# Performance work log

Hardware: AMD Instinct MI355X
Metric: run time of the kernel (lower is better)

The kernel has to match this reference:

```python
import jax, jax.numpy as jnp
import numpy as np
from jax import lax

TOP_N = 4
CAT_NUM = 4
IOU_THRESH = 0.25
PAD = 224
OUT_SZ = 224


def _gen_edge_anchors():
    # Faithful port of NTSNet._generate_default_anchor_maps for 448x448 input.
    settings = (
        dict(stride=32, size=48, scale=[2 ** (1.0 / 3.0), 2 ** (2.0 / 3.0)], ar=[0.667, 1, 1.5]),
        dict(stride=64, size=96, scale=[2 ** (1.0 / 3.0), 2 ** (2.0 / 3.0)], ar=[0.667, 1, 1.5]),
        dict(stride=128, size=192, scale=[1, 2 ** (1.0 / 3.0), 2 ** (2.0 / 3.0)], ar=[0.667, 1, 1.5]),
    )
    inp = np.array([448, 448], dtype=np.float32)
    edges = []
    for s in settings:
        stride = s['stride']
        oh, ow = np.ceil(inp / stride).astype(int)
        ostart = stride / 2.0
        oy = np.arange(ostart, ostart + stride * oh, stride, dtype=np.float32).reshape(oh, 1)
        ox = np.arange(ostart, ostart + stride * ow, stride, dtype=np.float32).reshape(1, ow)
        cy = np.broadcast_to(oy, (oh, ow)); cx = np.broadcast_to(ox, (oh, ow))
        for sc in s['scale']:
            for ar in s['ar']:
                h = s['size'] * sc / float(ar) ** 0.5
                w = s['size'] * sc * float(ar) ** 0.5
                e = np.stack([cy - h / 2.0, cx - w / 2.0, cy + h / 2.0, cx + w / 2.0], axis=-1).reshape(-1, 4)
                edges.append(e)
    return np.concatenate(edges, 0).astype(np.float32)

EDGE_ANCHORS = (_gen_edge_anchors() + PAD).astype(np.int32)  # [1614,4] (y0,x0,y1,x1) in padded coords
BOXES_F = jnp.asarray(EDGE_ANCHORS, jnp.float32)
BOXES_I = jnp.asarray(EDGE_ANCHORS, jnp.int32)
AREAS = (BOXES_F[:, 2] - BOXES_F[:, 0]) * (BOXES_F[:, 3] - BOXES_F[:, 1])
N_ANCHORS = EDGE_ANCHORS.shape[0]  # 1614


def _nms_single(scores):
    # Greedy hard NMS: pick top score, suppress IoU >= thresh, repeat TOP_N times.
    def step(valid, _):
        s = jnp.where(valid, scores, -jnp.inf)
        i = jnp.argmax(s)
        b = BOXES_F[i]
        sy = jnp.maximum(BOXES_F[:, 0], b[0]); sx = jnp.maximum(BOXES_F[:, 1], b[1])
        ey = jnp.minimum(BOXES_F[:, 2], b[2]); ex = jnp.minimum(BOXES_F[:, 3], b[3])
        ly = ey - sy; lx = ex - sx
        inter = jnp.where((ly < 0) | (lx < 0), 0.0, ly * lx)
        iou = inter / (AREAS + AREAS[i] - inter)
        return valid & (iou < IOU_THRESH), i
    _, idx = lax.scan(step, jnp.ones((N_ANCHORS,), bool), None, length=TOP_N)
    return idx  # [TOP_N] int


def _crop_resize(img, box):
    # img: [3, 896, 896]; box: int [4] = (y0,x0,y1,x1); bilinear, align_corners=True -> [3,224,224]
    hmax = img.shape[-1] - 1
    y0, x0, y1, x1 = box[0], box[1], box[2], box[3]
    t = jnp.arange(OUT_SZ, dtype=jnp.float32) / (OUT_SZ - 1.0)
    ys = y0.astype(jnp.float32) + t * (y1 - y0 - 1).astype(jnp.float32)
    xs = x0.astype(jnp.float32) + t * (x1 - x0 - 1).astype(jnp.float32)
    yf = jnp.floor(ys); xf = jnp.floor(xs)
    wy = (ys - yf)[None, :, None]; wx = (xs - xf)[None, None, :]
    yl = yf.astype(jnp.int32); yh = jnp.minimum(yl + 1, hmax)
    xl = xf.astype(jnp.int32); xh = jnp.minimum(xl + 1, hmax)
    g = lambda yi, xi: img[:, yi[:, None], xi[None, :]]
    top = g(yl, xl) * (1.0 - wx) + g(yl, xh) * wx
    bot = g(yh, xl) * (1.0 - wx) + g(yh, xh) * wx
    return top * (1.0 - wy) + bot * wy


def _conv(x, w, b, stride, pad):
    y = lax.conv_general_dilated(x, w, (stride, stride), ((pad, pad), (pad, pad)),
                                 dimension_numbers=('NCHW', 'OIHW', 'NCHW'))
    return y + b[None, :, None, None]


def _forward(x, bb_w, bb_b, w1, b1, t1w, t1b, w2, b2, t2w, t2b, w3, b3, t3w, t3b, cw, cb):
    B = x.shape[0]
    backbone = lambda z: jax.nn.relu(_conv(z, bb_w, bb_b, 32, 0))
    raw_pre = backbone(x)  # [B,2048,14,14]
    # Navigator unit
    y1 = jax.nn.relu(_conv(raw_pre, w1, b1, 1, 1))                                  # [B,128,14,14]
    z1 = (jnp.einsum('bchw,oc->bohw', y1, t1w) + t1b[None, :, None, None]).reshape(B, -1)
    y2 = jax.nn.relu(_conv(y1, w2, b2, 2, 1))                                        # [B,128,7,7]
    z2 = (jnp.einsum('bchw,oc->bohw', y2, t2w) + t2b[None, :, None, None]).reshape(B, -1)
    y3 = jax.nn.relu(_conv(y2, w3, b3, 2, 1))                                        # [B,128,4,4]
    z3 = (jnp.einsum('bchw,oc->bohw', y3, t3w) + t3b[None, :, None, None]).reshape(B, -1)
    rpn_score = jnp.concatenate([z1, z2, z3], axis=1)  # [B,1614]
    top_idx = jax.vmap(_nms_single)(rpn_score)          # [B,TOP_N]
    boxes = BOXES_I[top_idx]                            # [B,TOP_N,4]
    x_pad = jnp.pad(x, ((0, 0), (0, 0), (PAD, PAD), (PAD, PAD)))  # [B,3,896,896]
    parts = jax.vmap(lambda img, bs: jax.vmap(lambda b: _crop_resize(img, b))(bs))(x_pad, boxes)
    parts = lax.stop_gradient(parts).reshape(B * TOP_N, 3, OUT_SZ, OUT_SZ)  # .detach() in torch
    part_feat = backbone(parts).mean(axis=(2, 3)).reshape(B, TOP_N, 2048)
    part_feat = part_feat[:, :CAT_NUM].reshape(B, -1)   # [B,8192]
    raw_feat = lax.stop_gradient(raw_pre).mean(axis=(2, 3))  # [B,2048] (detached in torch)
    concat = jnp.concatenate([part_feat, raw_feat], axis=1)  # [B,10240]
    return concat @ cw.T + cb                           # [B,200]


def setup_inputs() -> dict:
    key = jax.random.key(0)
    ks = jax.random.split(key, 12)
    def w(k, shape, fan_in):
        return jax.random.normal(k, shape, jnp.float32) * np.float32(np.sqrt(2.0 / fan_in))
    return {
        'x': jax.random.normal(ks[0], (8, 3, 448, 448), jnp.float32),
        'bb_w': w(ks[1], (2048, 3, 32, 32), 3 * 32 * 32), 'bb_b': jnp.zeros((2048,), jnp.float32),
        'w1': w(ks[2], (128, 2048, 3, 3), 2048 * 9), 'b1': jnp.zeros((128,), jnp.float32),
        't1w': w(ks[3], (6, 128), 128), 't1b': jnp.zeros((6,), jnp.float32),
        'w2': w(ks[4], (128, 128, 3, 3), 128 * 9), 'b2': jnp.zeros((128,), jnp.float32),
        't2w': w(ks[5], (6, 128), 128), 't2b': jnp.zeros((6,), jnp.float32),
        'w3': w(ks[6], (128, 128, 3, 3), 128 * 9), 'b3': jnp.zeros((128,), jnp.float32),
        't3w': w(ks[7], (9, 128), 128), 't3b': jnp.zeros((9,), jnp.float32),
        'cw': w(ks[8], (200, 2048 * (CAT_NUM + 1)), 2048 * (CAT_NUM + 1)),
        'cb': jnp.zeros((200,), jnp.float32),
    }


def reference(x, bb_w, bb_b, w1, b1, t1w, t1b, w2, b2, t2w, t2b, w3, b3, t3w, t3b, cw, cb):
    return _forward(x, bb_w, bb_b, w1, b1, t1w, t1b, w2, b2, t2w, t2b, w3, b3, t3w, t3b, cw, cb)
```

## Files before the change

kernel.cpp:

```cpp
#include <hip/hip_runtime.h>
#include <math.h>


typedef _Float16 h8 __attribute__((ext_vector_type(8)));
typedef float f32x4 __attribute__((ext_vector_type(4)));

#define ASCALE 256.0f
#define WSCALE 16384.0f
#define RSCALE (1.0f / (256.0f * 16384.0f))

__device__ __forceinline__ void gload16(const void* g, void* l) {
  __builtin_amdgcn_global_load_lds(
      (__attribute__((address_space(1))) void*)(void*)(uintptr_t)g,
      (__attribute__((address_space(3))) void*)l, 16, 0, 0);
}

__global__ __launch_bounds__(256) void anchors_kernel(int* __restrict__ anch,
                                                      float* __restrict__ areas) {
  int i = blockIdx.x * 256 + threadIdx.x;
  if (i >= 1614) return;
  int stride, oh, a, pos;
  double size, sc;
  const double C13 = 1.2599210498948732;
  const double C23 = 1.5874010519681994;
  if (i < 1176) {
    stride = 32; size = 48.0; oh = 14; a = i / 196; pos = i % 196;
    sc = (a / 3 == 0) ? C13 : C23;
  } else if (i < 1470) {
    int r = i - 1176; stride = 64; size = 96.0; oh = 7; a = r / 49; pos = r % 49;
    sc = (a / 3 == 0) ? C13 : C23;
  } else {
    int r = i - 1470; stride = 128; size = 192.0; oh = 4; a = r / 16; pos = r % 16;
    int si = a / 3;
    sc = (si == 0) ? 1.0 : ((si == 1) ? C13 : C23);
  }
  int ari = a % 3;
  double ar = (ari == 0) ? 0.667 : ((ari == 1) ? 1.0 : 1.5);
  int gy = pos / oh, gx = pos % oh;
  float cy = 0.5f * (float)stride + (float)(stride * gy);
  float cx = 0.5f * (float)stride + (float)(stride * gx);
  double ss = sqrt(ar);
  double hd = (size * sc) / ss;
  double wd = (size * sc) * ss;
  float hh = (float)(hd * 0.5), wh = (float)(wd * 0.5);
  float e0 = (cy - hh) + 224.0f;
  float e1 = (cx - wh) + 224.0f;
  float e2 = (cy + hh) + 224.0f;
  float e3 = (cx + wh) + 224.0f;
  int y0 = (int)e0, x0 = (int)e1, y1i = (int)e2, x1i = (int)e3;
  anch[i * 4 + 0] = y0; anch[i * 4 + 1] = x0;
  anch[i * 4 + 2] = y1i; anch[i * 4 + 3] = x1i;
  areas[i] = (float)(y1i - y0) * (float)(x1i - x0);
}

__global__ __launch_bounds__(256) void permute_w(const float* __restrict__ w,
                                                 float* __restrict__ wp,
                                                 int Cout, int Cin) {
  int idx = blockIdx.x * 256 + threadIdx.x;
  int total = Cout * 9 * Cin;
  if (idx >= total) return;
  int c = idx % Cin; int t2 = idx / Cin; int tap = t2 % 9; int o = t2 / 9;
  wp[idx] = w[(o * Cin + c) * 9 + tap];
}

__global__ __launch_bounds__(256) void split_w(const float* __restrict__ src,
                                               _Float16* __restrict__ h,
                                               _Float16* __restrict__ l, int n8) {
  int i = blockIdx.x * 256 + threadIdx.x;
  if (i >= n8) return;
  float4 v0 = *(const float4*)(src + (size_t)i * 8);
  float4 v1 = *(const float4*)(src + (size_t)i * 8 + 4);
  float vv[8] = {v0.x, v0.y, v0.z, v0.w, v1.x, v1.y, v1.z, v1.w};
  h8 vh, vl;
#pragma unroll
  for (int j = 0; j < 8; ++j) {
    float s = vv[j] * WSCALE;
    _Float16 a = (_Float16)s;
    vh[j] = a; vl[j] = (_Float16)(s - (float)a);
  }
  *(h8*)(h + (size_t)i * 8) = vh;
  *(h8*)(l + (size_t)i * 8) = vl;
}

__global__ __launch_bounds__(256) void split_x(const float* __restrict__ x,
                                               _Float16* __restrict__ Ah,
                                               _Float16* __restrict__ Al) {
  int i = blockIdx.x * 256 + threadIdx.x;
  if (i >= 1664 * 384) return;
  int kq = i % 384, m = i / 384;
  int k = kq * 8;
  h8 vh = {}, vl = {};
  if (m < 1568) {
    int b = m / 196, pos = m % 196;
    int c = k >> 10, r = (k >> 5) & 31, col = k & 31;
    int py = (pos / 14) * 32 + r, px = (pos % 14) * 32 + col;
    const float* sp2 = x + (((size_t)(b * 3 + c) * 448 + py) * 448 + px);
    float4 v0 = *(const float4*)sp2;
    float4 v1 = *(const float4*)(sp2 + 4);
    float vv[8] = {v0.x, v0.y, v0.z, v0.w, v1.x, v1.y, v1.z, v1.w};
#pragma unroll
    for (int j = 0; j < 8; ++j) {
      float s = vv[j] * ASCALE;
      _Float16 a = (_Float16)s;
      vh[j] = a; vl[j] = (_Float16)(s - (float)a);
    }
  }
  *(h8*)(Ah + (size_t)m * 3072 + k) = vh;
  *(h8*)(Al + (size_t)m * 3072 + k) = vl;
}

__global__ __launch_bounds__(256) void gemm_bb_mfma(
    const _Float16* __restrict__ Ah, const _Float16* __restrict__ Al,
    const _Float16* __restrict__ Bh, const _Float16* __restrict__ Bl,
    float* __restrict__ P) {
  __shared__ __align__(16) char lds[32768];
  const int t = threadIdx.x;
  const int m0 = blockIdx.x * 128, n0 = blockIdx.y * 128;
  const int kz = blockIdx.z;
  const int lane = t & 63, w = t >> 6;
  const int wm = (w >> 1) * 64, wn = (w & 1) * 64;
  const int lrow = lane & 15, kg = lane >> 4;

  int offA[4], offB[4];
#pragma unroll
  for (int i = 0; i < 4; ++i) {
    int ba = (wm + i * 16 + lrow) * 64 + kg * 16;
    offA[i] = ba ^ (((ba >> 7) & 3) << 4);
    int bb2 = (wn + i * 16 + lrow) * 64 + kg * 16;
    offB[i] = bb2 ^ (((bb2 >> 7) & 3) << 4);
  }
  size_t gAo[2], gBo[2];
  int ldso[2];
#pragma unroll
  for (int e = 0; e < 2; ++e) {
    int p = e * 256 + t;
    int lsl = p ^ ((p >> 3) & 3);
    int row = lsl >> 2, kq = lsl & 3;
    gAo[e] = (size_t)(m0 + row) * 3072 + kq * 8;
    gBo[e] = (size_t)(n0 + row) * 3072 + kq * 8;
    ldso[e] = e * 4096 + (t & 192) * 16;
  }

  f32x4 acc[4][4] = {};
  const int kbeg = kz * 1536, kend = kbeg + 1536;
  for (int k0 = kbeg; k0 < kend; k0 += 32) {
#pragma unroll
    for (int e = 0; e < 2; ++e) {
      gload16(Ah + gAo[e] + k0, lds + ldso[e]);
      gload16(Al + gAo[e] + k0, lds + 8192 + ldso[e]);
      gload16(Bh + gBo[e] + k0, lds + 16384 + ldso[e]);
      gload16(Bl + gBo[e] + k0, lds + 24576 + ldso[e]);
    }
    __syncthreads();
    h8 fah[4], fal[4], fbh[4], fbl[4];
#pragma unroll
    for (int i = 0; i < 4; ++i) {
      fah[i] = *(const h8*)(lds + offA[i]);
      fal[i] = *(const h8*)(lds + 8192 + offA[i]);
      fbh[i] = *(const h8*)(lds + 16384 + offB[i]);
      fbl[i] = *(const h8*)(lds + 24576 + offB[i]);
    }
#pragma unroll
    for (int i = 0; i < 4; ++i)
#pragma unroll
      for (int j = 0; j < 4; ++j)
        acc[i][j] = __builtin_amdgcn_mfma_f32_16x16x32_f16(fah[i], fbh[j], acc[i][j], 0, 0, 0);
#pragma unroll
    for (int i = 0; i < 4; ++i)
#pragma unroll
      for (int j = 0; j < 4; ++j)
        acc[i][j] = __builtin_amdgcn_mfma_f32_16x16x32_f16(fah[i], fbl[j], acc[i][j], 0, 0, 0);
#pragma unroll
    for (int i = 0; i < 4; ++i)
#pragma unroll
      for (int j = 0; j < 4; ++j)
        acc[i][j] = __builtin_amdgcn_mfma_f32_16x16x32_f16(fal[i], fbh[j], acc[i][j], 0, 0, 0);
    __syncthreads();
  }
  float* Pz = P + (size_t)kz * 1664 * 2048;
  const int prow = (lane >> 4) * 4;
#pragma unroll
  for (int i = 0; i < 4; ++i) {
#pragma unroll
    for (int j = 0; j < 4; ++j) {
      int n = n0 + wn + j * 16 + lrow;
#pragma unroll
      for (int r = 0; r < 4; ++r) {
        int m = m0 + wm + i * 16 + prow + r;
        Pz[(size_t)m * 2048 + n] = acc[i][j][r];
      }
    }
  }
}

template <int WRITE_SPLIT>
__global__ __launch_bounds__(256) void bb_reduce(const float* __restrict__ P,
                                                 const float* __restrict__ bias,
                                                 float* __restrict__ raw,
                                                 _Float16* __restrict__ h,
                                                 _Float16* __restrict__ l) {
  int idx = blockIdx.x * 256 + threadIdx.x;
  int m = idx >> 8, col = (idx & 255) * 8;
  if (WRITE_SPLIT) {
    if (m >= 1664) return;
    if (m >= 1568) {
      h8 z = {};
      *(h8*)(h + (size_t)m * 2048 + col) = z;
      *(h8*)(l + (size_t)m * 2048 + col) = z;
      return;
    }
  } else {
    if (m >= 1568) return;
  }
  size_t o = (size_t)m * 2048 + col;
  const float* p0 = P + o;
  const float* p1 = P + (size_t)1664 * 2048 + o;
  float4 a0 = *(const float4*)(p0);
  float4 a1 = *(const float4*)(p0 + 4);
  float4 c0 = *(const float4*)(p1);
  float4 c1 = *(const float4*)(p1 + 4);
  float4 b0 = *(const float4*)(bias + col);
  float4 b1 = *(const float4*)(bias + col + 4);
  float v[8];
  v[0] = fmaxf(fmaf(a0.x + c0.x, RSCALE, b0.x), 0.f);
  v[1] = fmaxf(fmaf(a0.y + c0.y, RSCALE, b0.y), 0.f);
  v[2] = fmaxf(fmaf(a0.z + c0.z, RSCALE, b0.z), 0.f);
  v[3] = fmaxf(fmaf(a0.w + c0.w, RSCALE, b0.w), 0.f);
  v[4] = fmaxf(fmaf(a1.x + c1.x, RSCALE, b1.x), 0.f);
  v[5] = fmaxf(fmaf(a1.y + c1.y, RSCALE, b1.y), 0.f);
  v[6] = fmaxf(fmaf(a1.z + c1.z, RSCALE, b1.z), 0.f);
  v[7] = fmaxf(fmaf(a1.w + c1.w, RSCALE, b1.w), 0.f);
  *(float4*)(raw + o) = make_float4(v[0], v[1], v[2], v[3]);
  *(float4*)(raw + o + 4) = make_float4(v[4], v[5], v[6], v[7]);
  if (WRITE_SPLIT) {
    h8 vh, vl;
#pragma unroll
    for (int j = 0; j < 8; ++j) {
      float s = v[j] * ASCALE;
      _Float16 a = (_Float16)s;
      vh[j] = a; vl[j] = (_Float16)(s - (float)a);
    }
    *(h8*)(h + o) = vh;
    *(h8*)(l + o) = vl;
  }
}

__global__ __launch_bounds__(256) void gemm_nav_mfma(
    const _Float16* __restrict__ Ah, const _Float16* __restrict__ Al,
    const _Float16* __restrict__ Bh, const _Float16* __restrict__ Bl,
    float* __restrict__ part) {
  __shared__ __align__(16) char lds[32768];
  const int t = threadIdx.x;
  const int m0 = blockIdx.x * 128;
  const int sp = blockIdx.y;
  const int lane = t & 63, w = t >> 6;
  const int wm = (w >> 1) * 64, wn = (w & 1) * 64;
  const int lrow = lane & 15, kg = lane >> 4;

  int offA[4], offB[4];
#pragma unroll
  for (int i = 0; i < 4; ++i) {
    int ba = (wm + i * 16 + lrow) * 64 + kg * 16;
    offA[i] = ba ^ (((ba >> 7) & 3) << 4);
    int bb2 = (wn + i * 16 + lrow) * 64 + kg * 16;
    offB[i] = bb2 ^ (((bb2 >> 7) & 3) << 4);
  }
  size_t gBo[2];
  int ldso[2], akq8[2], ab[2], apy[2], apx[2], amv[2];
#pragma unroll
  for (int e = 0; e < 2; ++e) {
    int p = e * 256 + t;
    int lsl = p ^ ((p >> 3) & 3);
    int row = lsl >> 2, kq = lsl & 3;
    gBo[e] = (size_t)row * 18432 + kq * 8;
    ldso[e] = e * 4096 + (t & 192) * 16;
    int m = m0 + row;
    amv[e] = (m < 1568);
    int b = m / 196, pos = m % 196;
    ab[e] = b; apy[e] = pos / 14; apx[e] = pos % 14;
    akq8[e] = kq * 8;
  }

  f32x4 acc[4][4] = {};
  const int kbeg = sp * 576, kend = kbeg + 576;
  for (int k0 = kbeg; k0 < kend; k0 += 32) {
    const int tap = k0 >> 11;
    const int c = k0 & 2047;
    const int dy = tap / 3 - 1, dx = tap % 3 - 1;
#pragma unroll
    for (int e = 0; e < 2; ++e) {
      int sy = apy[e] + dy, sx = apx[e] + dx;
      bool ok = amv[e] && ((unsigned)sy < 14u) && ((unsigned)sx < 14u);
      size_t rowi = ok ? (size_t)(ab[e] * 196 + sy * 14 + sx) : (size_t)1600;
      size_t ao = rowi * 2048 + c + akq8[e];
      gload16(Ah + ao, lds + ldso[e]);
      gload16(Al + ao, lds + 8192 + ldso[e]);
      gload16(Bh + gBo[e] + k0, lds + 16384 + ldso[e]);
      gload16(Bl + gBo[e] + k0, lds + 24576 + ldso[e]);
    }
    __syncthreads();
    h8 fah[4], fal[4], fbh[4], fbl[4];
#pragma unroll
    for (int i = 0; i < 4; ++i) {
      fah[i] = *(const h8*)(lds + offA[i]);
      fal[i] = *(const h8*)(lds + 8192 + offA[i]);
      fbh[i] = *(const h8*)(lds + 16384 + offB[i]);
      fbl[i] = *(const h8*)(lds + 24576 + offB[i]);
    }
#pragma unroll
    for (int i = 0; i < 4; ++i)
#pragma unroll
      for (int j = 0; j < 4; ++j)
        acc[i][j] = __builtin_amdgcn_mfma_f32_16x16x32_f16(fah[i], fbh[j], acc[i][j], 0, 0, 0);
#pragma unroll
    for (int i = 0; i < 4; ++i)
#pragma unroll
      for (int j = 0; j < 4; ++j)
        acc[i][j] = __builtin_amdgcn_mfma_f32_16x16x32_f16(fah[i], fbl[j], acc[i][j], 0, 0, 0);
#pragma unroll
    for (int i = 0; i < 4; ++i)
#pragma unroll
      for (int j = 0; j < 4; ++j)
        acc[i][j] = __builtin_amdgcn_mfma_f32_16x16x32_f16(fal[i], fbh[j], acc[i][j], 0, 0, 0);
    __syncthreads();
  }
  const int prow = (lane >> 4) * 4;
#pragma unroll
  for (int i = 0; i < 4; ++i) {
#pragma unroll
    for (int j = 0; j < 4; ++j) {
      int n = wn + j * 16 + lrow;
#pragma unroll
      for (int r = 0; r < 4; ++r) {
        int m = m0 + wm + i * 16 + prow + r;
        if (m < 1568)
          part[((size_t)sp * 1568 + m) * 128 + n] = acc[i][j][r] * RSCALE;
      }
    }
  }
}

__global__ __launch_bounds__(256) void y1_reduce(const float* __restrict__ part,
                                                 const float* __restrict__ b1,
                                                 float* __restrict__ y1) {
  int idx = blockIdx.x * 256 + threadIdx.x;
  if (idx >= 1568 * 128) return;
  int o = idx & 127;
  float s = b1[o];
#pragma unroll
  for (int sp = 0; sp < 32; ++sp) s += part[(size_t)sp * 1568 * 128 + idx];
  y1[idx] = fmaxf(s, 0.f);
}

__global__ __launch_bounds__(256) void conv3x3s2(const float* __restrict__ in,
                                                 const float* __restrict__ wp,
                                                 const float* __restrict__ bias,
                                                 float* __restrict__ out,
                                                 int Hin, int Hout) {
  int idx = blockIdx.x * 256 + threadIdx.x;
  int total = 8 * Hout * Hout * 128;
  if (idx >= total) return;
  int o = idx & 127; int pos = idx >> 7;
  int ox = pos % Hout; int t2 = pos / Hout; int oy = t2 % Hout; int b = t2 / Hout;
  float acc = bias[o];
  for (int dy = 0; dy < 3; ++dy) {
    int iy = 2 * oy - 1 + dy;
    if (iy < 0 || iy >= Hin) continue;
    for (int dx = 0; dx < 3; ++dx) {
      int ix = 2 * ox - 1 + dx;
      if (ix < 0 || ix >= Hin) continue;
      const float* ip = in + ((b * Hin + iy) * Hin + ix) * 128;
      const float* wgt = wp + (o * 9 + dy * 3 + dx) * 128;
#pragma unroll 4
      for (int c = 0; c < 128; c += 4) {
        float4 a = *(const float4*)(ip + c);
        float4 ww = *(const float4*)(wgt + c);
        acc += a.x * ww.x + a.y * ww.y + a.z * ww.z + a.w * ww.w;
      }
    }
  }
  out[idx] = fmaxf(acc, 0.f);
}

__global__ __launch_bounds__(256) void scores_kernel(
    const float* __restrict__ y1, const float* __restrict__ y2,
    const float* __restrict__ y3, const float* __restrict__ t1w,
    const float* __restrict__ t1b, const float* __restrict__ t2w,
    const float* __restrict__ t2b, const float* __restrict__ t3w,
    const float* __restrict__ t3b, float* __restrict__ scores) {
  int idx = blockIdx.x * 256 + threadIdx.x;
  if (idx >= 8 * 1614) return;
  int b = idx / 1614, sI = idx % 1614;
  const float* f; const float* w; float bias;
  if (sI < 1176) {
    int a = sI / 196;
    f = y1 + (b * 196 + (sI % 196)) * 128; w = t1w + a * 128; bias = t1b[a];
  } else if (sI < 1470) {
    int r = sI - 1176; int a = r / 49;
    f = y2 + (b * 49 + (r % 49)) * 128; w = t2w + a * 128; bias = t2b[a];
  } else {
    int r = sI - 1470; int a = r / 16;
    f = y3 + (b * 16 + (r % 16)) * 128; w = t3w + a * 128; bias = t3b[a];
  }
  float acc = 0.f;
  for (int c = 0; c < 128; c += 4) {
    float4 a4 = *(const float4*)(f + c);
    float4 w4 = *(const float4*)(w + c);
    acc += a4.x * w4.x + a4.y * w4.y + a4.z * w4.z + a4.w * w4.w;
  }
  scores[idx] = acc + bias;
}

__global__ __launch_bounds__(256) void nms_kernel(const float* __restrict__ scores,
                                                  const int* __restrict__ anch,
                                                  const float* __restrict__ areas,
                                                  int* __restrict__ boxes) {
  const int b = blockIdx.x, t = threadIdx.x;
  const float* s = scores + b * 1614;
  __shared__ unsigned char valid[1614];
  __shared__ float rv[256];
  __shared__ int ri[256];
  for (int i = t; i < 1614; i += 256) valid[i] = 1;
  __syncthreads();
  for (int n = 0; n < 4; ++n) {
    float best = -INFINITY; int bi = 0x7fffffff;
    for (int i = t; i < 1614; i += 256) {
      if (valid[i]) {
        float v = s[i];
        if (v > best || (v == best && i < bi)) { best = v; bi = i; }
      }
    }
    rv[t] = best; ri[t] = bi;
    __syncthreads();
    for (int off = 128; off > 0; off >>= 1) {
      if (t < off) {
        float ov = rv[t + off]; int oi = ri[t + off];
        if (ov > rv[t] || (ov == rv[t] && oi < ri[t])) { rv[t] = ov; ri[t] = oi; }
      }
      __syncthreads();
    }
    int sel = ri[0];
    if (sel > 1613) sel = 0;
    const int4 bb = ((const int4*)anch)[sel];
    const float Ai = areas[sel];
    if (t == 0) ((int4*)boxes)[b * 4 + n] = bb;
    __syncthreads();
    for (int i = t; i < 1614; i += 256) {
      if (!valid[i]) continue;
      const int4 ab = ((const int4*)anch)[i];
      float sy = fmaxf((float)ab.x, (float)bb.x);
      float sx = fmaxf((float)ab.y, (float)bb.y);
      float ey = fminf((float)ab.z, (float)bb.z);
      float ex = fminf((float)ab.w, (float)bb.w);
      float ly = ey - sy, lx = ex - sx;
      float inter = (ly < 0.f || lx < 0.f) ? 0.f : ly * lx;
      float iou = inter / (areas[i] + Ai - inter);
      if (iou >= 0.25f) valid[i] = 0;
    }
    __syncthreads();
  }
}

__global__ __launch_bounds__(256) void crop_kernel(const float* __restrict__ x,
                                                   const int* __restrict__ boxes,
                                                   _Float16* __restrict__ Ah,
                                                   _Float16* __restrict__ Al) {
  int idx = blockIdx.x * 256 + threadIdx.x;
  if (idx >= 32 * 3 * 224 * 224) return;
  int px = idx % 224; int t1 = idx / 224; int py = t1 % 224; int t2 = t1 / 224;
  int c = t2 % 3; int p = t2 / 3;
  int b = p >> 2;
  const int4 bb = ((const int4*)boxes)[p];
  float ty = (float)py / 223.0f;
  float txf = (float)px / 223.0f;
  float ys = (float)bb.x + ty * (float)(bb.z - bb.x - 1);
  float xs = (float)bb.y + txf * (float)(bb.w - bb.y - 1);
  float yf = floorf(ys), xf = floorf(xs);
  float wy = ys - yf, wx = xs - xf;
  int yl = (int)yf, xl = (int)xf;
  int yh = min(yl + 1, 895), xh = min(xl + 1, 895);
  const float* img = x + (size_t)(b * 3 + c) * 448 * 448;
  auto samp = [&](int yy, int xx) -> float {
    yy -= 224; xx -= 224;
    if (yy < 0 || yy >= 448 || xx < 0 || xx >= 448) return 0.f;
    return img[yy * 448 + xx];
  };
  float v00 = samp(yl, xl), v01 = samp(yl, xh);
  float v10 = samp(yh, xl), v11 = samp(yh, xh);
  float top = v00 * (1.f - wx) + v01 * wx;
  float bot = v10 * (1.f - wx) + v11 * wx;
  float val = top * (1.f - wy) + bot * wy;
  int i = py >> 5, r = py & 31, j = px >> 5, col = px & 31;
  int m = p * 49 + i * 7 + j;
  int k = (c << 10) + (r << 5) + col;
  float s = val * ASCALE;
  _Float16 a = (_Float16)s;
  Ah[(size_t)m * 3072 + k] = a;
  Al[(size_t)m * 3072 + k] = (_Float16)(s - (float)a);
}

__global__ __launch_bounds__(256) void mean_kernel(const float* __restrict__ in,
                                                   float* __restrict__ out,
                                                   int rows) {
  int g = blockIdx.x >> 3;
  int o = ((blockIdx.x & 7) << 8) + threadIdx.x;
  const float* base = in + ((size_t)g * rows) * 2048 + o;
  float s0 = 0.f, s1 = 0.f, s2 = 0.f, s3 = 0.f;
  int r = 0;
  for (; r + 4 <= rows; r += 4) {
    s0 += base[(size_t)(r + 0) * 2048];
    s1 += base[(size_t)(r + 1) * 2048];
    s2 += base[(size_t)(r + 2) * 2048];
    s3 += base[(size_t)(r + 3) * 2048];
  }
  for (; r < rows; ++r) s0 += base[(size_t)r * 2048];
  out[(size_t)g * 2048 + o] = ((s0 + s1) + (s2 + s3)) / (float)rows;
}

__global__ __launch_bounds__(256) void final_kernel(const float* __restrict__ pfeat,
                                                    const float* __restrict__ rfeat,
                                                    const float* __restrict__ cw,
                                                    const float* __restrict__ cb,
                                                    float* __restrict__ out) {
  int gw = (blockIdx.x * 256 + threadIdx.x) >> 6;
  int lane = threadIdx.x & 63;
  if (gw >= 1600) return;
  int b = gw / 200, j = gw % 200;
  const float* wr = cw + (size_t)j * 10240;
  const float* pf = pfeat + (size_t)b * 8192;
  float acc = 0.f;
  for (int k = lane * 4; k < 8192; k += 256) {
    float4 a = *(const float4*)(pf + k);
    float4 w = *(const float4*)(wr + k);
    acc += a.x * w.x + a.y * w.y + a.z * w.z + a.w * w.w;
  }
  const float* rf = rfeat + (size_t)b * 2048;
  const float* wr2 = wr + 8192;
  for (int k = lane * 4; k < 2048; k += 256) {
    float4 a = *(const float4*)(rf + k);
    float4 w = *(const float4*)(wr2 + k);
    acc += a.x * w.x + a.y * w.y + a.z * w.z + a.w * w.w;
  }
#pragma unroll
  for (int off = 32; off > 0; off >>= 1) acc += __shfl_down(acc, off, 64);
  if (lane == 0) out[b * 200 + j] = acc + cb[j];
}

extern "C" void kernel_launch(void* const* d_in, const int* in_sizes, int n_in,
                              void* d_out, int out_size, void* d_ws, size_t ws_size,
                              hipStream_t stream) {
  const float* x   = (const float*)d_in[0];
  const float* bbw = (const float*)d_in[1];
  const float* bbb = (const float*)d_in[2];
  const float* w1  = (const float*)d_in[3];
  const float* b1  = (const float*)d_in[4];
  const float* t1w = (const float*)d_in[5];
  const float* t1b = (const float*)d_in[6];
  const float* w2  = (const float*)d_in[7];
  const float* b2  = (const float*)d_in[8];
  const float* t2w = (const float*)d_in[9];
  const float* t2b = (const float*)d_in[10];
  const float* w3  = (const float*)d_in[11];
  const float* b3  = (const float*)d_in[12];
  const float* t3w = (const float*)d_in[13];
  const float* t3b = (const float*)d_in[14];
  const float* cw  = (const float*)d_in[15];
  const float* cb  = (const float*)d_in[16];
  float* out = (float*)d_out;

  char* p = (char*)d_ws;
  auto alloc = [&](size_t bytes) -> char* {
    char* r = p; p += (bytes + 255) & ~(size_t)255; return r;
  };
  int*      anch  = (int*)     alloc((size_t)1614 * 4 * 4);
  float*    areas = (float*)   alloc((size_t)1614 * 4);
  float*    w1p   = (float*)   alloc((size_t)128 * 18432 * 4);
  _Float16* bWh   = (_Float16*)alloc((size_t)2048 * 3072 * 2);
  _Float16* bWl   = (_Float16*)alloc((size_t)2048 * 3072 * 2);
  _Float16* w1h   = (_Float16*)alloc((size_t)128 * 18432 * 2);
  _Float16* w1l   = (_Float16*)alloc((size_t)128 * 18432 * 2);
  _Float16* Ahh   = (_Float16*)alloc((size_t)1664 * 3072 * 2);
  _Float16* All   = (_Float16*)alloc((size_t)1664 * 3072 * 2);
  _Float16* rawh  = (_Float16*)alloc((size_t)1664 * 2048 * 2);
  _Float16* rawl  = (_Float16*)alloc((size_t)1664 * 2048 * 2);
  float*    raw   = (float*)   alloc((size_t)1568 * 2048 * 4);
  float*    w2p   = (float*)   alloc((size_t)128 * 9 * 128 * 4);
  float*    w3p   = (float*)   alloc((size_t)128 * 9 * 128 * 4);
  char*     big   = alloc((size_t)2 * 1664 * 2048 * 4);
  float*    Pbuf  = (float*)big;
  float*    y1s   = (float*)big;
  float*    y1v   = (float*)   alloc((size_t)1568 * 128 * 4);
  float*    y2v   = (float*)   alloc((size_t)392 * 128 * 4);
  float*    y3v   = (float*)   alloc((size_t)128 * 128 * 4);
  float*    sc    = (float*)   alloc((size_t)8 * 1614 * 4);
  int*      boxes = (int*)     alloc((size_t)8 * 4 * 4 * 4);
  float*    pfeat = (float*)   alloc((size_t)32 * 2048 * 4);
  float*    rfeat = (float*)   alloc((size_t)8 * 2048 * 4);

  anchors_kernel<<<7, 256, 0, stream>>>(anch, areas);
  permute_w<<<(128 * 9 * 2048 + 255) / 256, 256, 0, stream>>>(w1, w1p, 128, 2048);
  permute_w<<<(128 * 9 * 128 + 255) / 256, 256, 0, stream>>>(w2, w2p, 128, 128);
  permute_w<<<(128 * 9 * 128 + 255) / 256, 256, 0, stream>>>(w3, w3p, 128, 128);
  split_w<<<(2048 * 3072 / 8 + 255) / 256, 256, 0, stream>>>(bbw, bWh, bWl, 2048 * 3072 / 8);
  split_w<<<(128 * 18432 / 8 + 255) / 256, 256, 0, stream>>>(w1p, w1h, w1l, 128 * 18432 / 8);
  split_x<<<(1664 * 384 + 255) / 256, 256, 0, stream>>>(x, Ahh, All);

  gemm_bb_mfma<<<dim3(13, 16, 2), 256, 0, stream>>>(Ahh, All, bWh, bWl, Pbuf);
  bb_reduce<1><<<1664, 256, 0, stream>>>(Pbuf, bbb, raw, rawh, rawl);
  gemm_nav_mfma<<<dim3(13, 32), 256, 0, stream>>>(rawh, rawl, w1h, w1l, y1s);
  y1_reduce<<<(1568 * 128 + 255) / 256, 256, 0, stream>>>(y1s, b1, y1v);
  mean_kernel<<<64, 256, 0, stream>>>(raw, rfeat, 196);
  conv3x3s2<<<(8 * 7 * 7 * 128 + 255) / 256, 256, 0, stream>>>(y1v, w2p, b2, y2v, 14, 7);
  conv3x3s2<<<(8 * 4 * 4 * 128 + 255) / 256, 256, 0, stream>>>(y2v, w3p, b3, y3v, 7, 4);
  scores_kernel<<<(8 * 1614 + 255) / 256, 256, 0, stream>>>(
      y1v, y2v, y3v, t1w, t1b, t2w, t2b, t3w, t3b, sc);
  nms_kernel<<<8, 256, 0, stream>>>(sc, anch, areas, boxes);
  crop_kernel<<<(32 * 3 * 224 * 224) / 256, 256, 0, stream>>>(x, boxes, Ahh, All);
  gemm_bb_mfma<<<dim3(13, 16, 2), 256, 0, stream>>>(Ahh, All, bWh, bWl, Pbuf);
  bb_reduce<0><<<1568, 256, 0, stream>>>(Pbuf, bbb, raw, rawh, rawl);
  mean_kernel<<<256, 256, 0, stream>>>(raw, pfeat, 49);
  final_kernel<<<400, 256, 0, stream>>>(pfeat, rfeat, cw, cb, out);
}
```

Before: 415.7 us.

## Double-buffer LDS in split-f16 MFMA GEMMs and remap blocks across XCDs

Both MFMA GEMM kernels (backbone and navigator conv) now use two 32 KB LDS buffers, so the global-to-LDS loads for the next K step are issued before the current step's MFMAs. This is meant to hide memory latency and drop one barrier per iteration. Block indices are also remapped so that tiles sharing operands land on the same XCD, which should improve L2 reuse. The cost is doubled LDS per block (64 KB), which may lower occupancy. The wait before reading the prefetched buffer relies on the trailing __syncthreads draining the async loads.

```diff
diff --git a/kernel.cpp b/kernel.cpp
--- a/kernel.cpp
+++ b/kernel.cpp
@@ -113,9 +113,11 @@
     const _Float16* __restrict__ Ah, const _Float16* __restrict__ Al,
     const _Float16* __restrict__ Bh, const _Float16* __restrict__ Bl,
     float* __restrict__ P) {
-  __shared__ __align__(16) char lds[32768];
+  __shared__ __align__(16) char lds[65536];
   const int t = threadIdx.x;
-  const int m0 = blockIdx.x * 128, n0 = blockIdx.y * 128;
+  const int bid = blockIdx.x + 13 * blockIdx.y;
+  const int orig = (bid & 7) * 26 + (bid >> 3);
+  const int m0 = (orig % 13) * 128, n0 = (orig / 13) * 128;
   const int kz = blockIdx.z;
   const int lane = t & 63, w = t >> 6;
   const int wm = (w >> 1) * 64, wn = (w & 1) * 64;
@@ -141,24 +143,32 @@
     ldso[e] = e * 4096 + (t & 192) * 16;
   }
 
+  auto STAGE = [&](int buf, int k0) {
+    char* L = lds + buf * 32768;
+#pragma unroll
+    for (int e = 0; e < 2; ++e) {
+      gload16(Ah + gAo[e] + k0, L + ldso[e]);
+      gload16(Al + gAo[e] + k0, L + 8192 + ldso[e]);
+      gload16(Bh + gBo[e] + k0, L + 16384 + ldso[e]);
+      gload16(Bl + gBo[e] + k0, L + 24576 + ldso[e]);
+    }
+  };
+
   f32x4 acc[4][4] = {};
   const int kbeg = kz * 1536, kend = kbeg + 1536;
+  STAGE(0, kbeg);
+  __syncthreads();
+  int cur = 0;
   for (int k0 = kbeg; k0 < kend; k0 += 32) {
-#pragma unroll
-    for (int e = 0; e < 2; ++e) {
-      gload16(Ah + gAo[e] + k0, lds + ldso[e]);
-      gload16(Al + gAo[e] + k0, lds + 8192 + ldso[e]);
-      gload16(Bh + gBo[e] + k0, lds + 16384 + ldso[e]);
-      gload16(Bl + gBo[e] + k0, lds + 24576 + ldso[e]);
-    }
-    __syncthreads();
+    if (k0 + 32 < kend) STAGE(cur ^ 1, k0 + 32);
+    const char* L = lds + cur * 32768;
     h8 fah[4], fal[4], fbh[4], fbl[4];
 #pragma unroll
     for (int i = 0; i < 4; ++i) {
-      fah[i] = *(const h8*)(lds + offA[i]);
-      fal[i] = *(const h8*)(lds + 8192 + offA[i]);
-      fbh[i] = *(const h8*)(lds + 16384 + offB[i]);
-      fbl[i] = *(const h8*)(lds + 24576 + offB[i]);
+      fah[i] = *(const h8*)(L + offA[i]);
+      fal[i] = *(const h8*)(L + 8192 + offA[i]);
+      fbh[i] = *(const h8*)(L + 16384 + offB[i]);
+      fbl[i] = *(const h8*)(L + 24576 + offB[i]);
     }
 #pragma unroll
     for (int i = 0; i < 4; ++i)
@@ -176,6 +186,7 @@
       for (int j = 0; j < 4; ++j)
         acc[i][j] = __builtin_amdgcn_mfma_f32_16x16x32_f16(fal[i], fbh[j], acc[i][j], 0, 0, 0);
     __syncthreads();
+    cur ^= 1;
   }
   float* Pz = P + (size_t)kz * 1664 * 2048;
   const int prow = (lane >> 4) * 4;
@@ -249,10 +260,12 @@
     const _Float16* __restrict__ Ah, const _Float16* __restrict__ Al,
     const _Float16* __restrict__ Bh, const _Float16* __restrict__ Bl,
     float* __restrict__ part) {
-  __shared__ __align__(16) char lds[32768];
+  __shared__ __align__(16) char lds[65536];
   const int t = threadIdx.x;
-  const int m0 = blockIdx.x * 128;
-  const int sp = blockIdx.y;
+  const int bid = blockIdx.x + 13 * blockIdx.y;
+  const int orig = (bid & 7) * 52 + (bid >> 3);
+  const int m0 = (orig % 13) * 128;
+  const int sp = orig / 13;
   const int lane = t & 63, w = t >> 6;
   const int wm = (w >> 1) * 64, wn = (w & 1) * 64;
   const int lrow = lane & 15, kg = lane >> 4;
@@ -281,31 +294,39 @@
     akq8[e] = kq * 8;
   }
 
-  f32x4 acc[4][4] = {};
-  const int kbeg = sp * 576, kend = kbeg + 576;
-  for (int k0 = kbeg; k0 < kend; k0 += 32) {
+  auto STAGE = [&](int buf, int k0) {
     const int tap = k0 >> 11;
     const int c = k0 & 2047;
     const int dy = tap / 3 - 1, dx = tap % 3 - 1;
+    char* L = lds + buf * 32768;
 #pragma unroll
     for (int e = 0; e < 2; ++e) {
       int sy = apy[e] + dy, sx = apx[e] + dx;
       bool ok = amv[e] && ((unsigned)sy < 14u) && ((unsigned)sx < 14u);
       size_t rowi = ok ? (size_t)(ab[e] * 196 + sy * 14 + sx) : (size_t)1600;
       size_t ao = rowi * 2048 + c + akq8[e];
-      gload16(Ah + ao, lds + ldso[e]);
-      gload16(Al + ao, lds + 8192 + ldso[e]);
-      gload16(Bh + gBo[e] + k0, lds + 16384 + ldso[e]);
-      gload16(Bl + gBo[e] + k0, lds + 24576 + ldso[e]);
-    }
-    __syncthreads();
+      gload16(Ah + ao, L + ldso[e]);
+      gload16(Al + ao, L + 8192 + ldso[e]);
+      gload16(Bh + gBo[e] + k0, L + 16384 + ldso[e]);
+      gload16(Bl + gBo[e] + k0, L + 24576 + ldso[e]);
+    }
+  };
+
+  f32x4 acc[4][4] = {};
+  const int kbeg = sp * 576, kend = kbeg + 576;
+  STAGE(0, kbeg);
+  __syncthreads();
+  int cur = 0;
+  for (int k0 = kbeg; k0 < kend; k0 += 32) {
+    if (k0 + 32 < kend) STAGE(cur ^ 1, k0 + 32);
+    const char* L = lds + cur * 32768;
     h8 fah[4], fal[4], fbh[4], fbl[4];
 #pragma unroll
     for (int i = 0; i < 4; ++i) {
-      fah[i] = *(const h8*)(lds + offA[i]);
-      fal[i] = *(const h8*)(lds + 8192 + offA[i]);
-      fbh[i] = *(const h8*)(lds + 16384 + offB[i]);
-      fbl[i] = *(const h8*)(lds + 24576 + offB[i]);
+      fah[i] = *(const h8*)(L + offA[i]);
+      fal[i] = *(const h8*)(L + 8192 + offA[i]);
+      fbh[i] = *(const h8*)(L + 16384 + offB[i]);
+      fbl[i] = *(const h8*)(L + 24576 + offB[i]);
     }
 #pragma unroll
     for (int i = 0; i < 4; ++i)
@@ -323,6 +344,7 @@
       for (int j = 0; j < 4; ++j)
         acc[i][j] = __builtin_amdgcn_mfma_f32_16x16x32_f16(fal[i], fbh[j], acc[i][j], 0, 0, 0);
     __syncthreads();
+    cur ^= 1;
   }
   const int prow = (lane >> 4) * 4;
 #pragma unroll
```

Result: faster. 391.5 us (-5.8%).
